# Kernel optimization log

Hardware: AMD Instinct MI355X
Metric: run time of the kernel (lower is better)

## Reference

```python
import math
import jax, jax.numpy as jnp
import numpy as np

SIN_DIM = 8
HEADS = 4
HID = 64
EMBED = 6 + 1 + 3 * SIN_DIM + 5 + 2  # 38


def _sinusoidal(v):
    # v: [N] -> [N, SIN_DIM], interleaved sin/cos as in torch.stack(...).flatten(-2)
    div = jnp.exp(jnp.arange(0, SIN_DIM, 2, dtype=jnp.float32) * (-math.log(10000.0) / SIN_DIM))
    scaled = v[:, None] * div  # [N, SIN_DIM//2]
    return jnp.stack([jnp.sin(scaled), jnp.cos(scaled)], axis=-1).reshape(v.shape[0], SIN_DIM)


def _feature_embed(x):
    nt = jnp.clip(x[:, 0].astype(jnp.int32), 0, 5)
    role = jnp.clip(x[:, 5].astype(jnp.int32), 0, 4)
    return jnp.concatenate([
        jax.nn.one_hot(nt, 6, dtype=x.dtype),
        jnp.log1p(x[:, 1])[:, None],
        _sinusoidal(x[:, 2]),
        _sinusoidal(x[:, 3]),
        _sinusoidal(x[:, 4] * 100.0),
        jax.nn.one_hot(role, 5, dtype=x.dtype),
        x[:, 6:7],
        x[:, 7:8],
    ], axis=-1)  # [N, 38]


def _gat(x, adj, W, a_src, a_dst, concat):
    N = x.shape[0]
    h = (x @ W).reshape(N, HEADS, HID)                       # [N,H,D]
    src = jnp.einsum('nhd,hd->nh', h, a_src)                 # [N,H]
    dst = jnp.einsum('nhd,hd->nh', h, a_dst)                 # [N,H]
    e = src[:, None, :] + dst[None, :, :]                    # [N,N,H]
    e = jnp.where(e > 0, e, 0.2 * e)                         # leaky_relu(0.2)
    e = jnp.where(adj[:, :, None] > 0, e, -jnp.inf)
    a = jax.nn.softmax(e, axis=1)                            # softmax over neighbors j
    out = jnp.einsum('njh,nhd->nhd'.replace('nj', 'ij').replace('nhd,', 'jhd,').replace('->nhd', '->ihd'), a, h) if False else jnp.einsum('ijh,jhd->ihd', a, h)
    if concat:
        return out.reshape(N, HEADS * HID)
    return out.mean(axis=1)


def _layernorm(x, g, b, eps=1e-5):
    mu = x.mean(axis=-1, keepdims=True)
    var = ((x - mu) ** 2).mean(axis=-1, keepdims=True)
    return (x - mu) / jnp.sqrt(var + eps) * g + b


def setup_inputs() -> dict:
    key = jax.random.key(0)
    ks = jax.random.split(key, 16)
    N, C = 4096, 512
    # raw node features per FeatureEmbedding docstring
    nt = jax.random.randint(ks[0], (N,), 0, 6).astype(jnp.float32)
    arity = jax.random.randint(ks[1], (N,), 0, 5).astype(jnp.float32)
    arg_pos = jax.random.randint(ks[2], (N,), 0, 8).astype(jnp.float32)
    depth = jax.random.randint(ks[3], (N,), 0, 12).astype(jnp.float32)
    age = jax.random.uniform(ks[4], (N,))
    role = jax.random.randint(ks[5], (N,), 0, 5).astype(jnp.float32)
    pol = jax.random.bernoulli(ks[6], 0.5, (N,)).astype(jnp.float32)
    eq = jax.random.bernoulli(ks[7], 0.2, (N,)).astype(jnp.float32)
    node_features = jnp.stack([nt, arity, arg_pos, depth, age, role, pol, eq], axis=-1)
    adj = (jax.random.uniform(ks[8], (N, N)) < 0.01).astype(jnp.float32)
    adj = jnp.maximum(adj, jnp.eye(N, dtype=jnp.float32))  # self-loops
    pm = (jax.random.uniform(ks[9], (C, N)) < (8.0 / N)).astype(jnp.float32)
    pool_matrix = pm / jnp.clip(pm.sum(axis=1, keepdims=True), 1.0, None)
    def xavier(k, shape):
        fan = shape[0] + shape[-1]
        return jax.random.normal(k, shape, dtype=jnp.float32) * math.sqrt(2.0 / fan)
    return {
        'node_features': node_features, 'adj': adj, 'pool_matrix': pool_matrix,
        'W1': xavier(ks[10], (EMBED, HID * HEADS)),
        'a_src1': xavier(ks[11], (HEADS, HID)), 'a_dst1': xavier(ks[12], (HEADS, HID)),
        'g1': jnp.ones((HID * HEADS,), jnp.float32), 'b1': jnp.zeros((HID * HEADS,), jnp.float32),
        'W2': xavier(ks[13], (HID * HEADS, HID * HEADS)),
        'a_src2': xavier(ks[14], (HEADS, HID)), 'a_dst2': xavier(ks[15], (HEADS, HID)),
        'g2': jnp.ones((HID,), jnp.float32), 'b2': jnp.zeros((HID,), jnp.float32),
        'Ws': xavier(jax.random.fold_in(key, 100), (HID, HID)), 'bs': jnp.zeros((HID,), jnp.float32),
        'Wo': xavier(jax.random.fold_in(key, 101), (HID, 1)), 'bo': jnp.zeros((1,), jnp.float32),
    }


def reference(node_features, adj, pool_matrix, W1, a_src1, a_dst1, g1, b1,
              W2, a_src2, a_dst2, g2, b2, Ws, bs, Wo, bo):
    x = _feature_embed(node_features)                         # [N, 38]
    # layer 1: concat heads -> [N, 256]
    x = jax.nn.elu(_layernorm(_gat(x, adj, W1, a_src1, a_dst1, True), g1, b1))
    # layer 2: mean over heads -> [N, 64]  (dropout is eval-mode no-op)
    x = jax.nn.elu(_layernorm(_gat(x, adj, W2, a_src2, a_dst2, False), g2, b2))
    clause_emb = pool_matrix @ x                               # [C, 64]
    h = jax.nn.relu(clause_emb @ Ws + bs)                      # MLP scorer
    return (h @ Wo + bo)[:, 0]                                 # [C]
```

## Files before the change

### kernel.cpp

```cpp
#include <hip/hip_runtime.h>
#include <math.h>

#define N 4096
#define C 512
#define EMB 38
#define HEADS 4
#define HID 64
#define F1 256
#define MAXN 128
#define RPB 8

__device__ __forceinline__ float wr_sum(float v) {
#pragma unroll
    for (int o = 32; o > 0; o >>= 1) v += __shfl_xor(v, o);
    return v;
}
__device__ __forceinline__ float wr_max(float v) {
#pragma unroll
    for (int o = 32; o > 0; o >>= 1) v = fmaxf(v, __shfl_xor(v, o));
    return v;
}

__global__ __launch_bounds__(256) void k_build(const float* __restrict__ adj,
                                               int* __restrict__ cnt, int* __restrict__ idx) {
    int i = blockIdx.x, tid = threadIdx.x;
    int wv = tid >> 6, lane = tid & 63;
    __shared__ int wcnt[4];
    const float* row = adj + (size_t)i * N;
    float v[16];
#pragma unroll
    for (int k = 0; k < 16; ++k) v[k] = row[wv * 1024 + k * 64 + lane];
    unsigned long long m[16];
    int tot = 0;
#pragma unroll
    for (int k = 0; k < 16; ++k) { m[k] = __ballot(v[k] > 0.f); tot += __popcll(m[k]); }
    if (lane == 0) wcnt[wv] = tot;
    __syncthreads();
    int base = 0;
#pragma unroll
    for (int w = 0; w < 4; ++w) if (w < wv) base += wcnt[w];
    int total = wcnt[0] + wcnt[1] + wcnt[2] + wcnt[3];
    unsigned long long below = (1ull << lane) - 1;
    int off = base;
#pragma unroll
    for (int k = 0; k < 16; ++k) {
        if (v[k] > 0.f) {
            int p = off + __popcll(m[k] & below);
            if (p < MAXN) idx[i * MAXN + p] = wv * 1024 + k * 64 + lane;
        }
        off += __popcll(m[k]);
    }
    if (tid == 0) cnt[i] = min(total, MAXN);
}

__global__ __launch_bounds__(256) void k_gemm1(const float* __restrict__ nf, const float* __restrict__ W1,
                                               const float* __restrict__ asrc, const float* __restrict__ adst,
                                               float* __restrict__ h1, float* __restrict__ s1, float* __restrict__ d1) {
    int n0 = blockIdx.x * RPB, tid = threadIdx.x;
    __shared__ float fs[RPB][8];
    __shared__ float xs[RPB][40];
    if (tid < RPB * 8) fs[tid >> 3][tid & 7] = nf[(size_t)n0 * 8 + tid];
    if (tid < RPB * 2) xs[tid >> 1][38 + (tid & 1)] = 0.f;
    __syncthreads();
    {
        int r = tid & 7;
        int t = tid >> 3;
        const float* f = fs[r];
        for (int pass = 0; pass < 2; ++pass, t += 32) {
            if (t >= EMB) break;
            float val;
            if (t < 6) { int nt = min(max((int)f[0], 0), 5); val = (t == nt) ? 1.f : 0.f; }
            else if (t == 6) val = log1pf(f[1]);
            else if (t < 31) {
                int q = (t - 7) & 7, s = (t - 7) >> 3, m = q >> 1;
                float base = (s == 0) ? f[2] : (s == 1) ? f[3] : f[4] * 100.f;
                float div = expf((2.f * m) * (-logf(10000.f) / 8.f));
                float sc = base * div;
                val = (q & 1) ? cosf(sc) : sinf(sc);
            }
            else if (t < 36) { int role = min(max((int)f[5], 0), 4); val = (t - 31 == role) ? 1.f : 0.f; }
            else val = (t == 36) ? f[6] : f[7];
            xs[r][t] = val;
        }
    }
    __syncthreads();
    float acc[RPB];
#pragma unroll
    for (int r = 0; r < RPB; ++r) acc[r] = 0.f;
#pragma unroll
    for (int kk = 0; kk < 9; ++kk) {
        float w0 = W1[(4 * kk + 0) * F1 + tid];
        float w1 = W1[(4 * kk + 1) * F1 + tid];
        float w2 = W1[(4 * kk + 2) * F1 + tid];
        float w3 = W1[(4 * kk + 3) * F1 + tid];
#pragma unroll
        for (int r = 0; r < RPB; ++r) {
            float4 x = *(const float4*)&xs[r][4 * kk];
            acc[r] = fmaf(x.x, w0, fmaf(x.y, w1, fmaf(x.z, w2, fmaf(x.w, w3, acc[r]))));
        }
    }
#pragma unroll
    for (int k = 36; k < EMB; ++k) {
        float wvv = W1[k * F1 + tid];
#pragma unroll
        for (int r = 0; r < RPB; ++r) acc[r] = fmaf(xs[r][k], wvv, acc[r]);
    }
    int h = tid >> 6, lane = tid & 63;
    float av = asrc[tid], dv = adst[tid];
#pragma unroll
    for (int r = 0; r < RPB; ++r) {
        h1[(size_t)(n0 + r) * F1 + tid] = acc[r];
        float ss = wr_sum(acc[r] * av);
        float dd = wr_sum(acc[r] * dv);
        if (lane == 0) { s1[(n0 + r) * HEADS + h] = ss; d1[(n0 + r) * HEADS + h] = dd; }
    }
}

__global__ __launch_bounds__(256) void k_agg1(const float* __restrict__ h1, const float* __restrict__ s1,
                                              const float* __restrict__ d1, const int* __restrict__ cnt,
                                              const int* __restrict__ idx, const float* __restrict__ g,
                                              const float* __restrict__ b, float* __restrict__ xo) {
    int i = blockIdx.x, tid = threadIdx.x;
    int wv = tid >> 6, lane = tid & 63;
    __shared__ int nbrs[MAXN];
    __shared__ float wts[HEADS][MAXN + 1];
    __shared__ float lsum[HEADS];
    __shared__ float sacc[4][F1];
    __shared__ float red[HEADS];
    int c = cnt[i];
    if (tid < c) nbrs[tid] = idx[i * MAXN + tid];
    __syncthreads();
    if (tid < c) {
        float4 dd = ((const float4*)d1)[nbrs[tid]];
        float4 ss = ((const float4*)s1)[i];
        float e0 = ss.x + dd.x, e1 = ss.y + dd.y, e2 = ss.z + dd.z, e3 = ss.w + dd.w;
        wts[0][tid] = e0 > 0.f ? e0 : 0.2f * e0;
        wts[1][tid] = e1 > 0.f ? e1 : 0.2f * e1;
        wts[2][tid] = e2 > 0.f ? e2 : 0.2f * e2;
        wts[3][tid] = e3 > 0.f ? e3 : 0.2f * e3;
    }
    __syncthreads();
    {
        float m = -INFINITY;
        for (int jj = lane; jj < c; jj += 64) m = fmaxf(m, wts[wv][jj]);
        m = wr_max(m);
        float l = 0.f;
        for (int jj = lane; jj < c; jj += 64) { float t = expf(wts[wv][jj] - m); wts[wv][jj] = t; l += t; }
        l = wr_sum(l);
        if (lane == 0) lsum[wv] = l;
    }
    __syncthreads();
    int hq = lane >> 4;
    const float4* hv = (const float4*)h1;
    float4 acc = {0.f, 0.f, 0.f, 0.f};
    int jj = wv;
    for (; jj + 12 < c; jj += 16) {
        int na = nbrs[jj], nb = nbrs[jj + 4], nc = nbrs[jj + 8], nd = nbrs[jj + 12];
        float wa = wts[hq][jj], wb = wts[hq][jj + 4], wc = wts[hq][jj + 8], wd = wts[hq][jj + 12];
        float4 va = hv[(size_t)na * 64 + lane];
        float4 vb = hv[(size_t)nb * 64 + lane];
        float4 vc = hv[(size_t)nc * 64 + lane];
        float4 vd = hv[(size_t)nd * 64 + lane];
        acc.x = fmaf(wa, va.x, acc.x); acc.y = fmaf(wa, va.y, acc.y);
        acc.z = fmaf(wa, va.z, acc.z); acc.w = fmaf(wa, va.w, acc.w);
        acc.x = fmaf(wb, vb.x, acc.x); acc.y = fmaf(wb, vb.y, acc.y);
        acc.z = fmaf(wb, vb.z, acc.z); acc.w = fmaf(wb, vb.w, acc.w);
        acc.x = fmaf(wc, vc.x, acc.x); acc.y = fmaf(wc, vc.y, acc.y);
        acc.z = fmaf(wc, vc.z, acc.z); acc.w = fmaf(wc, vc.w, acc.w);
        acc.x = fmaf(wd, vd.x, acc.x); acc.y = fmaf(wd, vd.y, acc.y);
        acc.z = fmaf(wd, vd.z, acc.z); acc.w = fmaf(wd, vd.w, acc.w);
    }
    for (; jj < c; jj += 4) {
        int na = nbrs[jj];
        float wa = wts[hq][jj];
        float4 va = hv[(size_t)na * 64 + lane];
        acc.x = fmaf(wa, va.x, acc.x); acc.y = fmaf(wa, va.y, acc.y);
        acc.z = fmaf(wa, va.z, acc.z); acc.w = fmaf(wa, va.w, acc.w);
    }
    ((float4*)&sacc[wv][0])[lane] = acc;
    __syncthreads();
    float tot = (sacc[0][tid] + sacc[1][tid] + sacc[2][tid] + sacc[3][tid]) / lsum[wv];
    float s = wr_sum(tot);
    if (lane == 0) red[wv] = s;
    __syncthreads();
    float mu = (red[0] + red[1] + red[2] + red[3]) * (1.f / F1);
    float dvv = tot - mu;
    float s2 = wr_sum(dvv * dvv);
    __syncthreads();
    if (lane == 0) red[wv] = s2;
    __syncthreads();
    float var = (red[0] + red[1] + red[2] + red[3]) * (1.f / F1);
    float y = dvv * rsqrtf(var + 1e-5f) * g[tid] + b[tid];
    xo[(size_t)i * F1 + tid] = y > 0.f ? y : expm1f(y);
}

__global__ __launch_bounds__(256) void k_gemm2(const float* __restrict__ x1, const float* __restrict__ W2,
                                               const float* __restrict__ asrc, const float* __restrict__ adst,
                                               float* __restrict__ h2, float* __restrict__ s2, float* __restrict__ d2) {
    int n0 = blockIdx.x * RPB, tid = threadIdx.x;
    __shared__ float4 xs4[RPB][F1 / 4];
    {
        int r = tid >> 5, kk = tid & 31;
        const float4* x1v = (const float4*)x1;
        xs4[r][kk]      = x1v[(size_t)(n0 + r) * 64 + kk];
        xs4[r][kk + 32] = x1v[(size_t)(n0 + r) * 64 + kk + 32];
    }
    __syncthreads();
    float acc[RPB];
#pragma unroll
    for (int r = 0; r < RPB; ++r) acc[r] = 0.f;
    for (int kk = 0; kk < F1 / 4; ++kk) {
        float w0 = W2[(4 * kk + 0) * F1 + tid];
        float w1 = W2[(4 * kk + 1) * F1 + tid];
        float w2 = W2[(4 * kk + 2) * F1 + tid];
        float w3 = W2[(4 * kk + 3) * F1 + tid];
#pragma unroll
        for (int r = 0; r < RPB; ++r) {
            float4 x = xs4[r][kk];
            acc[r] = fmaf(x.x, w0, fmaf(x.y, w1, fmaf(x.z, w2, fmaf(x.w, w3, acc[r]))));
        }
    }
    int h = tid >> 6, lane = tid & 63;
    float av = asrc[tid], dv = adst[tid];
#pragma unroll
    for (int r = 0; r < RPB; ++r) {
        h2[(size_t)(n0 + r) * F1 + tid] = acc[r];
        float ss = wr_sum(acc[r] * av);
        float dd = wr_sum(acc[r] * dv);
        if (lane == 0) { s2[(n0 + r) * HEADS + h] = ss; d2[(n0 + r) * HEADS + h] = dd; }
    }
}

__global__ __launch_bounds__(256) void k_agg2(const float* __restrict__ h2, const float* __restrict__ s2,
                                              const float* __restrict__ d2, const int* __restrict__ cnt,
                                              const int* __restrict__ idx, const float* __restrict__ g,
                                              const float* __restrict__ b, float* __restrict__ xo) {
    int i = blockIdx.x, tid = threadIdx.x;
    int wv = tid >> 6, lane = tid & 63;
    __shared__ int nbrs[MAXN];
    __shared__ float wts[HEADS][MAXN + 1];
    __shared__ float lsum[HEADS];
    __shared__ float sacc[4][F1];
    int c = cnt[i];
    if (tid < c) nbrs[tid] = idx[i * MAXN + tid];
    __syncthreads();
    if (tid < c) {
        float4 dd = ((const float4*)d2)[nbrs[tid]];
        float4 ss = ((const float4*)s2)[i];
        float e0 = ss.x + dd.x, e1 = ss.y + dd.y, e2 = ss.z + dd.z, e3 = ss.w + dd.w;
        wts[0][tid] = e0 > 0.f ? e0 : 0.2f * e0;
        wts[1][tid] = e1 > 0.f ? e1 : 0.2f * e1;
        wts[2][tid] = e2 > 0.f ? e2 : 0.2f * e2;
        wts[3][tid] = e3 > 0.f ? e3 : 0.2f * e3;
    }
    __syncthreads();
    {
        float m = -INFINITY;
        for (int jj = lane; jj < c; jj += 64) m = fmaxf(m, wts[wv][jj]);
        m = wr_max(m);
        float l = 0.f;
        for (int jj = lane; jj < c; jj += 64) { float t = expf(wts[wv][jj] - m); wts[wv][jj] = t; l += t; }
        l = wr_sum(l);
        if (lane == 0) lsum[wv] = l;
    }
    __syncthreads();
    int hq = lane >> 4;
    const float4* hvv = (const float4*)h2;
    float4 acc = {0.f, 0.f, 0.f, 0.f};
    int jj = wv;
    for (; jj + 12 < c; jj += 16) {
        int na = nbrs[jj], nb = nbrs[jj + 4], nc = nbrs[jj + 8], nd = nbrs[jj + 12];
        float wa = wts[hq][jj], wb = wts[hq][jj + 4], wc = wts[hq][jj + 8], wd = wts[hq][jj + 12];
        float4 va = hvv[(size_t)na * 64 + lane];
        float4 vb = hvv[(size_t)nb * 64 + lane];
        float4 vc = hvv[(size_t)nc * 64 + lane];
        float4 vd = hvv[(size_t)nd * 64 + lane];
        acc.x = fmaf(wa, va.x, acc.x); acc.y = fmaf(wa, va.y, acc.y);
        acc.z = fmaf(wa, va.z, acc.z); acc.w = fmaf(wa, va.w, acc.w);
        acc.x = fmaf(wb, vb.x, acc.x); acc.y = fmaf(wb, vb.y, acc.y);
        acc.z = fmaf(wb, vb.z, acc.z); acc.w = fmaf(wb, vb.w, acc.w);
        acc.x = fmaf(wc, vc.x, acc.x); acc.y = fmaf(wc, vc.y, acc.y);
        acc.z = fmaf(wc, vc.z, acc.z); acc.w = fmaf(wc, vc.w, acc.w);
        acc.x = fmaf(wd, vd.x, acc.x); acc.y = fmaf(wd, vd.y, acc.y);
        acc.z = fmaf(wd, vd.z, acc.z); acc.w = fmaf(wd, vd.w, acc.w);
    }
    for (; jj < c; jj += 4) {
        int na = nbrs[jj];
        float wa = wts[hq][jj];
        float4 va = hvv[(size_t)na * 64 + lane];
        acc.x = fmaf(wa, va.x, acc.x); acc.y = fmaf(wa, va.y, acc.y);
        acc.z = fmaf(wa, va.z, acc.z); acc.w = fmaf(wa, va.w, acc.w);
    }
    ((float4*)&sacc[wv][0])[lane] = acc;
    __syncthreads();
    if (wv == 0) {
        float t0 = 0.f, t1 = 0.f, t2 = 0.f, t3 = 0.f;
#pragma unroll
        for (int w = 0; w < 4; ++w) {
            t0 += sacc[w][lane];
            t1 += sacc[w][lane + 64];
            t2 += sacc[w][lane + 128];
            t3 += sacc[w][lane + 192];
        }
        float mv = (t0 / lsum[0] + t1 / lsum[1] + t2 / lsum[2] + t3 / lsum[3]) * 0.25f;
        float mu = wr_sum(mv) * (1.f / HID);
        float dvv = mv - mu;
        float var = wr_sum(dvv * dvv) * (1.f / HID);
        float y = dvv * rsqrtf(var + 1e-5f) * g[lane] + b[lane];
        xo[i * HID + lane] = y > 0.f ? y : expm1f(y);
    }
}

__global__ __launch_bounds__(256) void k_poolscore(const float* __restrict__ pm, const float* __restrict__ x2,
                                                   const float* __restrict__ Ws, const float* __restrict__ bs,
                                                   const float* __restrict__ Wo, const float* __restrict__ bo,
                                                   float* __restrict__ out) {
    int c = blockIdx.x, tid = threadIdx.x;
    int w = tid >> 6, lane = tid & 63;
    __shared__ float sacc[4][HID];
    __shared__ float ce_s[HID];
    float acc = 0.f;
    const float4* pmv = (const float4*)(pm + (size_t)c * N);
#pragma unroll
    for (int it = 0; it < 4; ++it) {
        int vi = w * 256 + it * 64 + lane;
        float4 p4 = pmv[vi];
        float pc[4] = {p4.x, p4.y, p4.z, p4.w};
#pragma unroll
        for (int comp = 0; comp < 4; ++comp) {
            unsigned long long msk = __ballot(pc[comp] != 0.f);
            while (msk) {
                int bpos = __ffsll(msk) - 1;
                msk &= msk - 1;
                float pj = __shfl(pc[comp], bpos);
                int j = (w * 256 + it * 64 + bpos) * 4 + comp;
                acc += pj * x2[(size_t)j * HID + lane];
            }
        }
    }
    sacc[w][lane] = acc;
    __syncthreads();
    if (w == 0) ce_s[lane] = sacc[0][lane] + sacc[1][lane] + sacc[2][lane] + sacc[3][lane];
    __syncthreads();
    if (w == 0) {
        float hd = bs[lane];
#pragma unroll 8
        for (int k = 0; k < HID; ++k) hd = fmaf(ce_s[k], Ws[k * HID + lane], hd);
        hd = fmaxf(hd, 0.f);
        float v = wr_sum(hd * Wo[lane]);
        if (lane == 0) out[c] = v + bo[0];
    }
}

extern "C" void kernel_launch(void* const* d_in, const int* in_sizes, int n_in,
                              void* d_out, int out_size, void* d_ws, size_t ws_size,
                              hipStream_t stream) {
    const float* nf  = (const float*)d_in[0];
    const float* adj = (const float*)d_in[1];
    const float* pm  = (const float*)d_in[2];
    const float* W1  = (const float*)d_in[3];
    const float* as1 = (const float*)d_in[4];
    const float* ad1 = (const float*)d_in[5];
    const float* g1  = (const float*)d_in[6];
    const float* b1  = (const float*)d_in[7];
    const float* W2  = (const float*)d_in[8];
    const float* as2 = (const float*)d_in[9];
    const float* ad2 = (const float*)d_in[10];
    const float* g2  = (const float*)d_in[11];
    const float* b2  = (const float*)d_in[12];
    const float* Ws  = (const float*)d_in[13];
    const float* bs  = (const float*)d_in[14];
    const float* Wo  = (const float*)d_in[15];
    const float* bo  = (const float*)d_in[16];
    float* out = (float*)d_out;

    float* p = (float*)d_ws;
    float* h1  = p; p += (size_t)N * F1;
    float* s1  = p; p += (size_t)N * HEADS;
    float* d1  = p; p += (size_t)N * HEADS;
    float* x1  = p; p += (size_t)N * F1;
    float* h2  = p; p += (size_t)N * F1;
    float* s2  = p; p += (size_t)N * HEADS;
    float* d2  = p; p += (size_t)N * HEADS;
    float* x2  = p; p += (size_t)N * HID;
    int* cnt = (int*)p;
    int* idx = cnt + N;

    k_build<<<N, 256, 0, stream>>>(adj, cnt, idx);
    k_gemm1<<<N / RPB, 256, 0, stream>>>(nf, W1, as1, ad1, h1, s1, d1);
    k_agg1<<<N, 256, 0, stream>>>(h1, s1, d1, cnt, idx, g1, b1, x1);
    k_gemm2<<<N / RPB, 256, 0, stream>>>(x1, W2, as2, ad2, h2, s2, d2);
    k_agg2<<<N, 256, 0, stream>>>(h2, s2, d2, cnt, idx, g2, b2, x2);
    k_poolscore<<<C, 256, 0, stream>>>(pm, x2, Ws, bs, Wo, bo, out);
}
```

Before: 193.2 us.

## Split adjacency compaction into float4 bitmask pass and per-row scan kernel

```diff
diff --git a/kernel.cpp b/kernel.cpp
--- a/kernel.cpp
+++ b/kernel.cpp
@@ -9,6 +9,7 @@
 #define F1 256
 #define MAXN 128
 #define RPB 8
+#define NWAVES 8192
 
 __device__ __forceinline__ float wr_sum(float v) {
 #pragma unroll
@@ -21,36 +22,61 @@
     return v;
 }
 
-__global__ __launch_bounds__(256) void k_build(const float* __restrict__ adj,
-                                               int* __restrict__ cnt, int* __restrict__ idx) {
-    int i = blockIdx.x, tid = threadIdx.x;
+__global__ __launch_bounds__(256) void k_bits(const float* __restrict__ adj,
+                                              unsigned long long* __restrict__ bits) {
+    int tid = threadIdx.x;
     int wv = tid >> 6, lane = tid & 63;
-    __shared__ int wcnt[4];
-    const float* row = adj + (size_t)i * N;
-    float v[16];
-#pragma unroll
-    for (int k = 0; k < 16; ++k) v[k] = row[wv * 1024 + k * 64 + lane];
-    unsigned long long m[16];
-    int tot = 0;
-#pragma unroll
-    for (int k = 0; k < 16; ++k) { m[k] = __ballot(v[k] > 0.f); tot += __popcll(m[k]); }
-    if (lane == 0) wcnt[wv] = tot;
-    __syncthreads();
+    int wave = blockIdx.x * 4 + wv;
+    const float4* a4 = (const float4*)adj;
+    float4 v[8];
+#pragma unroll
+    for (int k = 0; k < 8; ++k)
+        v[k] = a4[(size_t)(wave + k * NWAVES) * 64 + lane];
+#pragma unroll
+    for (int k = 0; k < 8; ++k) {
+        int g = wave + k * NWAVES;
+        unsigned long long bx = __ballot(v[k].x > 0.f);
+        unsigned long long by = __ballot(v[k].y > 0.f);
+        unsigned long long bz = __ballot(v[k].z > 0.f);
+        unsigned long long bw = __ballot(v[k].w > 0.f);
+        unsigned long long mine = (lane == 0) ? bx : (lane == 1) ? by : (lane == 2) ? bz : bw;
+        if (lane < 4) bits[(size_t)g * 4 + lane] = mine;
+    }
+}
+
+__global__ __launch_bounds__(256) void k_compact(const unsigned long long* __restrict__ bits,
+                                                 int* __restrict__ cnt, int* __restrict__ idx) {
+    int tid = threadIdx.x;
+    int wv = tid >> 6, lane = tid & 63;
+    int row = blockIdx.x * 4 + wv;
+    unsigned long long u = bits[(size_t)row * 64 + lane];
     int base = 0;
 #pragma unroll
-    for (int w = 0; w < 4; ++w) if (w < wv) base += wcnt[w];
-    int total = wcnt[0] + wcnt[1] + wcnt[2] + wcnt[3];
-    unsigned long long below = (1ull << lane) - 1;
-    int off = base;
-#pragma unroll
-    for (int k = 0; k < 16; ++k) {
-        if (v[k] > 0.f) {
-            int p = off + __popcll(m[k] & below);
-            if (p < MAXN) idx[i * MAXN + p] = wv * 1024 + k * 64 + lane;
-        }
-        off += __popcll(m[k]);
-    }
-    if (tid == 0) cnt[i] = min(total, MAXN);
+    for (int g = 0; g < 16; ++g) {
+        unsigned long long mx = __shfl(u, 4 * g + 0);
+        unsigned long long my = __shfl(u, 4 * g + 1);
+        unsigned long long mz = __shfl(u, 4 * g + 2);
+        unsigned long long mw = __shfl(u, 4 * g + 3);
+        int b0 = (int)((mx >> lane) & 1ull);
+        int b1 = (int)((my >> lane) & 1ull);
+        int b2 = (int)((mz >> lane) & 1ull);
+        int b3 = (int)((mw >> lane) & 1ull);
+        int cn = b0 + b1 + b2 + b3;
+        int sc = cn;
+#pragma unroll
+        for (int o = 1; o < 64; o <<= 1) {
+            int t = __shfl_up(sc, o);
+            if (lane >= o) sc += t;
+        }
+        int p = base + sc - cn;
+        int col0 = g * 256 + 4 * lane;
+        if (b0) { if (p < MAXN) idx[row * MAXN + p] = col0;     ++p; }
+        if (b1) { if (p < MAXN) idx[row * MAXN + p] = col0 + 1; ++p; }
+        if (b2) { if (p < MAXN) idx[row * MAXN + p] = col0 + 2; ++p; }
+        if (b3) { if (p < MAXN) idx[row * MAXN + p] = col0 + 3; ++p; }
+        base += __shfl(sc, 63);
+    }
+    if (lane == 0) cnt[row] = min(base, MAXN);
 }
 
 __global__ __launch_bounds__(256) void k_gemm1(const float* __restrict__ nf, const float* __restrict__ W1,
@@ -385,8 +411,10 @@
     float* x2  = p; p += (size_t)N * HID;
     int* cnt = (int*)p;
     int* idx = cnt + N;
-
-    k_build<<<N, 256, 0, stream>>>(adj, cnt, idx);
+    unsigned long long* bits = (unsigned long long*)(idx + (size_t)N * MAXN);
+
+    k_bits<<<2048, 256, 0, stream>>>(adj, bits);
+    k_compact<<<N / 4, 256, 0, stream>>>(bits, cnt, idx);
     k_gemm1<<<N / RPB, 256, 0, stream>>>(nf, W1, as1, ad1, h1, s1, d1);
     k_agg1<<<N, 256, 0, stream>>>(h1, s1, d1, cnt, idx, g1, b1, x1);
     k_gemm2<<<N / RPB, 256, 0, stream>>>(x1, W2, as2, ad2, h2, s2, d2);
```

Result: slower. 214.0 us (+10.8%).
